# Kernel optimization log

Measured on AMD Instinct MI355X. Metric: run time of the kernel, lower is better.

Reference implementation:

```python
import jax, jax.numpy as jnp
import numpy as np
from functools import partial

# ---- constants from params ----
NODES = 64          # cfg_s[0]: nodes per graph
HEADS, BASES = 8, 4 # EGConv num_heads / num_bases (aggregators = ['symnorm'], A=1)
THRESH, LENS = 0.5, 0.5
ENC_THRESH, ENC_LENS = 0.5, 0.5
DECAY = 0.2
LSTM_ALPHA = 2.0

# ---- surrogate spike functions ----
@partial(jax.custom_vjp, nondiff_argnums=(1, 2))
def atan_spike(x, thresh, alpha):
    return (x > thresh).astype(x.dtype)

def _atan_fwd(x, thresh, alpha):
    return atan_spike(x, thresh, alpha), x

def _atan_bwd(thresh, alpha, x, g):
    grad = (alpha / 2.0) / (1.0 + (jnp.pi / 2.0 * alpha * (x - thresh)) ** 2)
    return (g * grad,)

atan_spike.defvjp(_atan_fwd, _atan_bwd)

@partial(jax.custom_vjp, nondiff_argnums=(1,))
def erf_spike(x, alpha):
    return (x > 0).astype(x.dtype)

def _erf_fwd(x, alpha):
    return erf_spike(x, alpha), x

def _erf_bwd(alpha, x, g):
    grad = alpha / (2.0 * jnp.sqrt(jnp.pi)) * jnp.exp(-(alpha * x / 2.0) ** 2)
    return (g * grad,)

erf_spike.defvjp(_erf_fwd, _erf_bwd)


def setup_inputs() -> dict:
    key = jax.random.key(0)
    N, Cin, T = 16384, 8, 32
    Cenc, Cgnn = 128, 128
    Fh = Cgnn // HEADS
    HID, FC1, NC = 512, 256, 4
    E = 262144
    ks = jax.random.split(key, 12)

    def w(k, shape, fan_in):
        return jax.random.normal(k, shape, jnp.float32) / np.float32(np.sqrt(fan_in))

    return {
        "x": jax.random.normal(ks[0], (N, Cin, T), jnp.float32),
        "edge_index": jax.random.randint(ks[1], (2, E), 0, N, dtype=jnp.int32),
        "enc_W": w(ks[2], (Cin, Cenc), Cin),
        "enc_b": jnp.zeros((Cenc,), jnp.float32),
        "bases_W": w(ks[3], (Cenc, BASES * Fh), Cenc),
        "bases_b": jnp.zeros((BASES * Fh,), jnp.float32),
        "comb_W": w(ks[4], (Cenc, HEADS * BASES), Cenc),
        "comb_b": jnp.zeros((HEADS * BASES,), jnp.float32),
        "conv_bias": jnp.zeros((Cgnn,), jnp.float32),
        "W_ih": w(ks[5], (NODES * Cgnn, 4 * HID), NODES * Cgnn),
        "W_hh": w(ks[6], (HID, 4 * HID), HID),
        "b_ih": jnp.zeros((4 * HID,), jnp.float32),
        "b_hh": jnp.zeros((4 * HID,), jnp.float32),
        "fc1_W": w(ks[7], (HID, FC1), HID),
        "fc1_b": jnp.zeros((FC1,), jnp.float32),
        "fc2_W": w(ks[8], (FC1, NC), FC1),
        "fc2_b": jnp.zeros((NC,), jnp.float32),
    }


def reference(x, edge_index, enc_W, enc_b, bases_W, bases_b, comb_W, comb_b,
              conv_bias, W_ih, W_hh, b_ih, b_hh, fc1_W, fc1_b, fc2_W, fc2_b):
    N, Cin, T = x.shape
    S = N // NODES
    Cgnn = conv_bias.shape[0]
    Fh = Cgnn // HEADS
    HID = W_hh.shape[0]
    FC1 = fc1_b.shape[0]
    NC = fc2_b.shape[0]

    # EGConv symnorm graph structure with self-loops (fixed across time)
    loop = jnp.arange(N, dtype=edge_index.dtype)
    s_all = jnp.concatenate([edge_index[0], loop])
    d_all = jnp.concatenate([edge_index[1], loop])
    deg = jax.ops.segment_sum(jnp.ones(s_all.shape[0], x.dtype), d_all, num_segments=N)
    dinv = jnp.where(deg > 0, jax.lax.rsqrt(jnp.maximum(deg, 1e-12)), 0.0)
    ew = dinv[s_all] * dinv[d_all]  # [E+N]

    xs = jnp.moveaxis(x, -1, 0)  # [T, N, Cin]

    def step(carry, xt):
        (enc_mem, enc_spike, c1_mem, c1_spike, lh, lc,
         h1_mem, h1_spike, h2_mem, h2_spike, h2_sum) = carry
        # encoding LIF
        enc_mem = enc_mem * DECAY * (1.0 - enc_spike) + xt @ enc_W + enc_b
        enc_spike = atan_spike(enc_mem, ENC_THRESH, ENC_LENS)
        # EGConv (symnorm aggregator, A=1)
        bases = enc_spike @ bases_W + bases_b                       # [N, B*Fh]
        agg = jax.ops.segment_sum(ew[:, None] * bases[s_all], d_all, num_segments=N)
        comb = (enc_spike @ comb_W + comb_b).reshape(N, HEADS, BASES)
        conv = jnp.einsum('nhb,nbf->nhf', comb, agg.reshape(N, BASES, Fh))
        conv = conv.reshape(S, NODES, Cgnn) + conv_bias
        # conv LIF
        c1_mem = c1_mem * DECAY * (1.0 - c1_spike) + conv
        c1_spike = atan_spike(c1_mem, THRESH, LENS)
        # spiking LSTM cell (erf surrogates on all gates)
        xl = c1_spike.reshape(S, NODES * Cgnn)
        gates = xl @ W_ih + b_ih + lh @ W_hh + b_hh
        i, f, g, o = jnp.split(gates, 4, axis=-1)
        i = erf_spike(i, LSTM_ALPHA)
        f = erf_spike(f, LSTM_ALPHA)
        g = erf_spike(g, LSTM_ALPHA)
        o = erf_spike(o, LSTM_ALPHA)
        lc = f * lc + i * g
        lh = lc * o
        # fc1 LIF
        h1_mem = h1_mem * DECAY * (1.0 - h1_spike) + lh @ fc1_W + fc1_b
        h1_spike = atan_spike(h1_mem, THRESH, LENS)
        # fc2 LIF
        h2_mem = h2_mem * DECAY * (1.0 - h2_spike) + h1_spike @ fc2_W + fc2_b
        h2_spike = atan_spike(h2_mem, THRESH, LENS)
        return (enc_mem, enc_spike, c1_mem, c1_spike, lh, lc,
                h1_mem, h1_spike, h2_mem, h2_spike, h2_sum + h2_spike), None

    Cenc = enc_b.shape[0]
    z = lambda shape: jnp.zeros(shape, x.dtype)
    carry0 = (z((N, Cenc)), z((N, Cenc)), z((S, NODES, Cgnn)), z((S, NODES, Cgnn)),
              z((S, HID)), z((S, HID)), z((S, FC1)), z((S, FC1)),
              z((S, NC)), z((S, NC)), z((S, NC)))
    carry, _ = jax.lax.scan(step, carry0, xs)
    h2_sum = carry[-1]
    return h2_sum / jnp.asarray(T, x.dtype)
```

## Files before the change

### kernel.cpp

```cpp
#include <hip/hip_runtime.h>

#define NN      16384
#define TSTEPS  32
#define SG      256
#define NE      262144
#define NPANEL  24
#define GSTRIDE 524288u

#define OFF_ENC_MEM   0u
#define OFF_ENC_SPK   2097152u
#define OFF_C1_MEM    4194304u
#define OFF_C1_SPK    6291456u
#define OFF_LH        8388608u
#define OFF_LC        8519680u
#define OFF_H1_MEM    8650752u
#define OFF_H1_SPK    8716288u
#define OFF_H2_MEM    8781824u
#define OFF_H2_SPK    8782848u
#define OFF_H2_SUM    8783872u
#define ZERO_FLOATS   8784896u
#define OFF_BASES     8784896u
#define OFF_COMB      9833472u
#define OFF_GATES     10357760u
#define OFF_PART      10882048u
#define OFF_DINV      23464960u
#define OFF_COLW      23481344u
#define FLOAT_END     23743488u
#define IOFF_DEG      0
#define IOFF_FILL     16384
#define IOFF_ROWPTR   32768
#define IOFF_EID      49153
#define IOFF_COL      311297
#define INT_COUNT     573441

__global__ void k_deg(const int* __restrict__ ei, int* __restrict__ deg) {
  int e = blockIdx.x * 256 + threadIdx.x;
  if (e < NE) atomicAdd(&deg[ei[NE + e]], 1);
}

__global__ void k_dinv(const int* __restrict__ deg, float* __restrict__ dinv) {
  int n = blockIdx.x * 256 + threadIdx.x;
  if (n < NN) dinv[n] = __fdiv_rn(1.0f, __fsqrt_rn((float)(deg[n] + 1)));
}

__global__ void k_scan(const int* __restrict__ deg, int* __restrict__ rowp) {
  __shared__ int sdata[1024];
  int tid = threadIdx.x;
  int base = tid * 16;
  int loc[16];
  int sum = 0;
  #pragma unroll
  for (int i = 0; i < 16; ++i) { loc[i] = sum; sum += deg[base + i]; }
  sdata[tid] = sum;
  __syncthreads();
  for (int off = 1; off < 1024; off <<= 1) {
    int v = 0;
    if (tid >= off) v = sdata[tid - off];
    __syncthreads();
    sdata[tid] += v;
    __syncthreads();
  }
  int excl = (tid == 0) ? 0 : sdata[tid - 1];
  #pragma unroll
  for (int i = 0; i < 16; ++i) rowp[base + i] = excl + loc[i];
  if (tid == 1023) rowp[NN] = sdata[1023];
}

__global__ void k_scatter(const int* __restrict__ ei, const int* __restrict__ rowp,
                          int* __restrict__ fill, int* __restrict__ eid) {
  int e = blockIdx.x * 256 + threadIdx.x;
  if (e >= NE) return;
  int d = ei[NE + e];
  int pos = rowp[d] + atomicAdd(&fill[d], 1);
  eid[pos] = e;
}

__global__ void k_sortadj(const int* __restrict__ rowp, int* __restrict__ eid,
                          const int* __restrict__ ei, const float* __restrict__ dinv,
                          int* __restrict__ col, float* __restrict__ colw) {
  int d = blockIdx.x * 256 + threadIdx.x;
  if (d >= NN) return;
  int r0 = rowp[d], r1 = rowp[d + 1];
  for (int i = r0 + 1; i < r1; ++i) {
    int key = eid[i];
    int j = i - 1;
    while (j >= r0 && eid[j] > key) { eid[j + 1] = eid[j]; --j; }
    eid[j + 1] = key;
  }
  for (int i = r0; i < r1; ++i) {
    int s = ei[eid[i]];
    col[i] = s;
    colw[i] = dinv[s];
  }
}

__global__ __launch_bounds__(256) void k_enc(
    const float* __restrict__ x, const float* __restrict__ encW, const float* __restrict__ encB,
    float* __restrict__ enc_mem, float* __restrict__ enc_spk, int t) {
  __shared__ float xs[2][8];
  int tid = threadIdx.x;
  int nb = blockIdx.x * 2;
  if (tid < 16)
    xs[tid >> 3][tid & 7] = x[(size_t)(nb + (tid >> 3)) * 256 + (size_t)(tid & 7) * 32 + t];
  __syncthreads();
  int nl = tid >> 7, j = tid & 127;
  int idx = (nb + nl) * 128 + j;
  float dot = 0.f;
  #pragma unroll
  for (int c = 0; c < 8; ++c) dot = __fmaf_rn(xs[nl][c], encW[c * 128 + j], dot);
  float m = enc_mem[idx], s = enc_spk[idx];
  float nm = __fadd_rn(__fadd_rn(__fmul_rn(__fmul_rn(m, 0.2f), __fsub_rn(1.f, s)), dot), encB[j]);
  enc_mem[idx] = nm;
  enc_spk[idx] = nm > 0.5f ? 1.f : 0.f;
}

__global__ __launch_bounds__(256) void k_bases_comb(
    const float* __restrict__ enc_spk,
    const float* __restrict__ basesW, const float* __restrict__ basesB,
    const float* __restrict__ combW, const float* __restrict__ combB,
    float* __restrict__ bases, float* __restrict__ comb) {
  __shared__ float sp[64 * 129];
  __shared__ float ob[64 * 65];
  __shared__ float oc[64 * 33];
  const int tid = threadIdx.x;
  const int nb = blockIdx.x * 64;
  #pragma unroll 4
  for (int k = 0; k < 32; ++k) {
    int idx = k * 256 + tid;
    int n = idx >> 7, j = idx & 127;
    sp[n * 129 + j] = enc_spk[(size_t)nb * 128 + idx];
  }
  __syncthreads();
  const int lane = tid & 63;
  const int w = tid >> 6;
  const float* spn = sp + lane * 129;
  if (w < 2) {
    const int ch0 = w * 32;
    const float* Wp = basesW + ch0;
    float acc[32];
    #pragma unroll
    for (int c = 0; c < 32; ++c) acc[c] = 0.f;
    for (int j = 0; j < 128; ++j) {
      const float s = spn[j];
      const float* wr = Wp + j * 64;
      #pragma unroll
      for (int c = 0; c < 32; ++c) acc[c] = __fmaf_rn(s, wr[c], acc[c]);
    }
    #pragma unroll
    for (int c = 0; c < 32; ++c) ob[lane * 65 + ch0 + c] = acc[c];
  } else {
    const int ch0 = (w - 2) * 16;
    const float* Wp = combW + ch0;
    float acc[16];
    #pragma unroll
    for (int c = 0; c < 16; ++c) acc[c] = 0.f;
    for (int j = 0; j < 128; ++j) {
      const float s = spn[j];
      const float* wr = Wp + j * 32;
      #pragma unroll
      for (int c = 0; c < 16; ++c) acc[c] = __fmaf_rn(s, wr[c], acc[c]);
    }
    #pragma unroll
    for (int c = 0; c < 16; ++c) oc[lane * 33 + ch0 + c] = acc[c];
  }
  __syncthreads();
  #pragma unroll
  for (int r = 0; r < 16; ++r) {
    int idx = r * 256 + tid;
    int n = idx >> 6, ch = idx & 63;
    bases[(size_t)(nb + n) * 64 + ch] = __fadd_rn(ob[n * 65 + ch], basesB[ch]);
  }
  #pragma unroll
  for (int r = 0; r < 8; ++r) {
    int idx = r * 256 + tid;
    int n = idx >> 5, ch = idx & 31;
    comb[(size_t)(nb + n) * 32 + ch] = __fadd_rn(oc[n * 33 + ch], combB[ch]);
  }
}

__global__ __launch_bounds__(256) void k_aggconv(
    const float* __restrict__ bases, const float* __restrict__ comb,
    const float* __restrict__ dinv, const int* __restrict__ rowp,
    const int* __restrict__ col, const float* __restrict__ colw,
    const float* __restrict__ convB,
    float* __restrict__ c1_mem, float* __restrict__ c1_spk) {
  __shared__ float aggl[4][64];
  __shared__ float combl[4][32];
  int w = threadIdx.x >> 6;
  int m = threadIdx.x & 63;
  int d = blockIdx.x * 4 + w;
  float dd = dinv[d];
  int r0 = rowp[d], r1 = rowp[d + 1];
  float acc = 0.f;
  for (int r = r0; r < r1; ++r) {
    int s = col[r];
    float ew  = __fmul_rn(colw[r], dd);
    float upd = __fmul_rn(ew, bases[(size_t)s * 64 + m]);
    acc = __fadd_rn(acc, upd);
  }
  {
    float ew  = __fmul_rn(dd, dd);
    float upd = __fmul_rn(ew, bases[(size_t)d * 64 + m]);
    acc = __fadd_rn(acc, upd);
  }
  aggl[w][m] = acc;
  if (m < 32) combl[w][m] = comb[(size_t)d * 32 + m];
  __syncthreads();
  #pragma unroll
  for (int half = 0; half < 2; ++half) {
    int j = m + half * 64;
    int h = j >> 4, f = j & 15;
    float cv = 0.f;
    #pragma unroll
    for (int b = 0; b < 4; ++b)
      cv = __fadd_rn(cv, __fmul_rn(combl[w][h * 4 + b], aggl[w][b * 16 + f]));
    cv = __fadd_rn(cv, convB[j]);
    int idx = d * 128 + j;
    float cm = c1_mem[idx], cs = c1_spk[idx];
    float nm = __fadd_rn(__fmul_rn(__fmul_rn(cm, 0.2f), __fsub_rn(1.f, cs)), cv);
    c1_mem[idx] = nm;
    c1_spk[idx] = nm > 0.5f ? 1.f : 0.f;
  }
}

__global__ __launch_bounds__(256) void k_gpanel(
    const float* __restrict__ xl, const float* __restrict__ lh,
    const float* __restrict__ Wih, const float* __restrict__ Whh,
    float* __restrict__ part) {
  __shared__ __align__(16) float Ast[16][132];
  __shared__ __align__(16) float Bs[16][132];
  const int tid = threadIdx.x;
  const int tx = tid & 15, ty = tid >> 4;
  const int n0 = blockIdx.x * 128;
  const int m0 = blockIdx.y * 128;
  const int z  = blockIdx.z;

  const float* Asrc; const float* Bsrc; int lda, k0, klen;
  if (z < 22) { Asrc = xl; Bsrc = Wih; lda = 8192; k0 = z * 384; klen = (z == 21) ? 128 : 384; }
  else        { Asrc = lh; Bsrc = Whh; lda = 512;  k0 = (z == 22) ? 0 : 384; klen = (z == 22) ? 384 : 128; }

  float acc[8][8];
  #pragma unroll
  for (int i = 0; i < 8; ++i)
    #pragma unroll
    for (int j = 0; j < 8; ++j) acc[i][j] = 0.f;

  const int arow = tid >> 1;
  const int acol = (tid & 1) * 8;
  const int brow = tid >> 5;
  const int bcol = (tid & 31) * 4;

  const int nkt = klen >> 4;
  for (int kt = 0; kt < nkt; ++kt) {
    const int kb = k0 + (kt << 4);
    __syncthreads();
    {
      const float* src = Asrc + (size_t)(m0 + arow) * lda + kb + acol;
      const float4 v0 = ((const float4*)src)[0];
      const float4 v1 = ((const float4*)src)[1];
      Ast[acol + 0][arow] = v0.x; Ast[acol + 1][arow] = v0.y;
      Ast[acol + 2][arow] = v0.z; Ast[acol + 3][arow] = v0.w;
      Ast[acol + 4][arow] = v1.x; Ast[acol + 5][arow] = v1.y;
      Ast[acol + 6][arow] = v1.z; Ast[acol + 7][arow] = v1.w;
    }
    {
      *(float4*)&Bs[brow][bcol] =
          *(const float4*)(Bsrc + (size_t)(kb + brow) * 2048 + n0 + bcol);
      *(float4*)&Bs[brow + 8][bcol] =
          *(const float4*)(Bsrc + (size_t)(kb + brow + 8) * 2048 + n0 + bcol);
    }
    __syncthreads();
    #pragma unroll
    for (int kk = 0; kk < 16; ++kk) {
      const float4 a0 = *(const float4*)&Ast[kk][ty * 4];
      const float4 a1 = *(const float4*)&Ast[kk][64 + ty * 4];
      const float4 b0 = *(const float4*)&Bs[kk][tx * 4];
      const float4 b1 = *(const float4*)&Bs[kk][64 + tx * 4];
      const float av[8] = {a0.x, a0.y, a0.z, a0.w, a1.x, a1.y, a1.z, a1.w};
      const float bv[8] = {b0.x, b0.y, b0.z, b0.w, b1.x, b1.y, b1.z, b1.w};
      #pragma unroll
      for (int i = 0; i < 8; ++i)
        #pragma unroll
        for (int j = 0; j < 8; ++j)
          acc[i][j] = __fmaf_rn(av[i], bv[j], acc[i][j]);
    }
  }
  float* dstz = part + (size_t)z * GSTRIDE + (size_t)m0 * 2048 + n0;
  #pragma unroll
  for (int i = 0; i < 8; ++i) {
    const int mr = ((i >> 2) << 6) + ty * 4 + (i & 3);
    float* row = dstz + (size_t)mr * 2048;
    *(float4*)(row + tx * 4)      = make_float4(acc[i][0], acc[i][1], acc[i][2], acc[i][3]);
    *(float4*)(row + 64 + tx * 4) = make_float4(acc[i][4], acc[i][5], acc[i][6], acc[i][7]);
  }
}

__global__ __launch_bounds__(256) void k_combine(
    const float* __restrict__ part, const float* __restrict__ bih,
    const float* __restrict__ bhh, float* __restrict__ gates) {
  const int idx = blockIdx.x * 256 + threadIdx.x;
  const float* p = part + idx;
  float tih = p[0];
  #pragma unroll
  for (int zz = 1; zz < 22; ++zz) tih = __fadd_rn(tih, p[(size_t)zz * GSTRIDE]);
  const float thh = __fadd_rn(p[22u * GSTRIDE], p[23u * GSTRIDE]);
  const int u = idx & 2047;
  gates[idx] = __fadd_rn(__fadd_rn(__fadd_rn(tih, bih[u]), thh), bhh[u]);
}

__global__ __launch_bounds__(256) void k_cell(
    const float* __restrict__ gates,
    float* __restrict__ lc, float* __restrict__ lh,
    const float* __restrict__ fc1W, const float* __restrict__ fc1b,
    const float* __restrict__ fc2W, const float* __restrict__ fc2b,
    float* __restrict__ h1_mem, float* __restrict__ h1_spk,
    float* __restrict__ h2_mem, float* __restrict__ h2_spk, float* __restrict__ h2_sum) {
  __shared__ float lhl[512];
  __shared__ float sp1l[256];
  const int s = blockIdx.x;
  const int p = threadIdx.x;
  #pragma unroll
  for (int half = 0; half < 2; ++half) {
    const int h = p + half * 256;
    const float giv = gates[(size_t)s * 2048 + h];
    const float gfv = gates[(size_t)s * 2048 + 512 + h];
    const float ggv = gates[(size_t)s * 2048 + 1024 + h];
    const float gov = gates[(size_t)s * 2048 + 1536 + h];
    const float iv = giv > 0.f ? 1.f : 0.f;
    const float fv = gfv > 0.f ? 1.f : 0.f;
    const float gv = ggv > 0.f ? 1.f : 0.f;
    const float ov = gov > 0.f ? 1.f : 0.f;
    const int li = s * 512 + h;
    const float lcv = __fadd_rn(__fmul_rn(fv, lc[li]), __fmul_rn(iv, gv));
    lc[li] = lcv;
    const float lhv = __fmul_rn(lcv, ov);
    lh[li] = lhv;
    lhl[h] = lhv;
  }
  __syncthreads();
  float a0 = 0.f, a1 = 0.f;
  #pragma unroll 8
  for (int q = 0; q < 384; ++q) a0 = __fmaf_rn(lhl[q], fc1W[q * 256 + p], a0);
  #pragma unroll 8
  for (int q = 384; q < 512; ++q) a1 = __fmaf_rn(lhl[q], fc1W[q * 256 + p], a1);
  const float dot1 = __fadd_rn(a0, a1);
  const int i1 = s * 256 + p;
  const float m1 = h1_mem[i1], s1o = h1_spk[i1];
  const float nm1 = __fadd_rn(__fadd_rn(__fmul_rn(__fmul_rn(m1, 0.2f), __fsub_rn(1.f, s1o)), dot1), fc1b[p]);
  h1_mem[i1] = nm1;
  const float sp1 = nm1 > 0.5f ? 1.f : 0.f;
  h1_spk[i1] = sp1;
  sp1l[p] = sp1;
  __syncthreads();
  if (p < 4) {
    float acc = 0.f;
    for (int q = 0; q < 256; ++q) acc = __fmaf_rn(sp1l[q], fc2W[q * 4 + p], acc);
    const int i2 = s * 4 + p;
    const float m2 = h2_mem[i2], s2o = h2_spk[i2];
    const float nm2 = __fadd_rn(__fadd_rn(__fmul_rn(__fmul_rn(m2, 0.2f), __fsub_rn(1.f, s2o)), acc), fc2b[p]);
    h2_mem[i2] = nm2;
    const float sp2 = nm2 > 0.5f ? 1.f : 0.f;
    h2_spk[i2] = sp2;
    h2_sum[i2] = __fadd_rn(h2_sum[i2], sp2);
  }
}

__global__ void k_out(const float* __restrict__ h2_sum, float* __restrict__ out) {
  int i = blockIdx.x * 256 + threadIdx.x;
  if (i < SG * 4) out[i] = __fmul_rn(h2_sum[i], 0.03125f);
}

extern "C" void kernel_launch(void* const* d_in, const int* in_sizes, int n_in,
                              void* d_out, int out_size, void* d_ws, size_t ws_size,
                              hipStream_t stream) {
  const float* x      = (const float*)d_in[0];
  const int*   ei     = (const int*)  d_in[1];
  const float* encW   = (const float*)d_in[2];
  const float* encB   = (const float*)d_in[3];
  const float* basesW = (const float*)d_in[4];
  const float* basesB = (const float*)d_in[5];
  const float* combW  = (const float*)d_in[6];
  const float* combB  = (const float*)d_in[7];
  const float* convB  = (const float*)d_in[8];
  const float* Wih    = (const float*)d_in[9];
  const float* Whh    = (const float*)d_in[10];
  const float* bih    = (const float*)d_in[11];
  const float* bhh    = (const float*)d_in[12];
  const float* fc1W   = (const float*)d_in[13];
  const float* fc1b   = (const float*)d_in[14];
  const float* fc2W   = (const float*)d_in[15];
  const float* fc2b   = (const float*)d_in[16];

  float* ws = (float*)d_ws;
  float* enc_mem = ws + OFF_ENC_MEM;
  float* enc_spk = ws + OFF_ENC_SPK;
  float* c1_mem  = ws + OFF_C1_MEM;
  float* c1_spk  = ws + OFF_C1_SPK;
  float* lhp     = ws + OFF_LH;
  float* lcp     = ws + OFF_LC;
  float* h1_mem  = ws + OFF_H1_MEM;
  float* h1_spk  = ws + OFF_H1_SPK;
  float* h2_mem  = ws + OFF_H2_MEM;
  float* h2_spk  = ws + OFF_H2_SPK;
  float* h2_sum  = ws + OFF_H2_SUM;
  float* bases   = ws + OFF_BASES;
  float* comb    = ws + OFF_COMB;
  float* gates   = ws + OFF_GATES;
  float* partp   = ws + OFF_PART;
  float* dinv    = ws + OFF_DINV;
  float* colw    = ws + OFF_COLW;
  int* ibase = (int*)((char*)d_ws + (size_t)FLOAT_END * 4);
  int* deg  = ibase + IOFF_DEG;
  int* fill = ibase + IOFF_FILL;
  int* rowp = ibase + IOFF_ROWPTR;
  int* eid  = ibase + IOFF_EID;
  int* col  = ibase + IOFF_COL;

  hipMemsetAsync(ws, 0, (size_t)ZERO_FLOATS * 4, stream);
  hipMemsetAsync(ibase, 0, 32768 * 4, stream);

  k_deg    <<<NE / 256, 256, 0, stream>>>(ei, deg);
  k_dinv   <<<NN / 256, 256, 0, stream>>>(deg, dinv);
  k_scan   <<<1, 1024, 0, stream>>>(deg, rowp);
  k_scatter<<<NE / 256, 256, 0, stream>>>(ei, rowp, fill, eid);
  k_sortadj<<<NN / 256, 256, 0, stream>>>(rowp, eid, ei, dinv, col, colw);

  for (int t = 0; t < TSTEPS; ++t) {
    k_enc       <<<NN / 2, 256, 0, stream>>>(x, encW, encB, enc_mem, enc_spk, t);
    k_bases_comb<<<NN / 64, 256, 0, stream>>>(enc_spk, basesW, basesB, combW, combB, bases, comb);
    k_aggconv   <<<NN / 4, 256, 0, stream>>>(bases, comb, dinv, rowp, col, colw, convB, c1_mem, c1_spk);
    k_gpanel    <<<dim3(16, 2, NPANEL), 256, 0, stream>>>(c1_spk, lhp, Wih, Whh, partp);
    k_combine   <<<2048, 256, 0, stream>>>(partp, bih, bhh, gates);
    k_cell      <<<SG, 256, 0, stream>>>(gates, lcp, lhp, fc1W, fc1b, fc2W, fc2b,
                                         h1_mem, h1_spk, h2_mem, h2_spk, h2_sum);
  }
  k_out<<<4, 256, 0, stream>>>(h2_sum, (float*)d_out);
}
```

Measured before the change: 7.218 ms.

## Fuse encoder LIF into bases kernel and stream GEMM B tiles through registers

The encoder LIF update now runs inside the bases/comb kernel. The spikes are written straight into shared memory, which removes one launch per timestep and a global re-read of enc_spk. The gate GEMM panel kernel now loads the W tiles directly from global memory into registers per thread instead of staging them in shared memory. It also halves the K tile to 8 and adds an occupancy hint of 3 blocks. This cuts LDS use and traffic, but each thread issues more uncoalesced-pattern global loads, the loop has more barrier iterations, and register pressure may rise.

```diff
diff --git a/kernel.cpp b/kernel.cpp
--- a/kernel.cpp
+++ b/kernel.cpp
@@ -94,41 +94,39 @@
   }
 }
 
-__global__ __launch_bounds__(256) void k_enc(
+__global__ __launch_bounds__(256) void k_encbases(
     const float* __restrict__ x, const float* __restrict__ encW, const float* __restrict__ encB,
-    float* __restrict__ enc_mem, float* __restrict__ enc_spk, int t) {
-  __shared__ float xs[2][8];
-  int tid = threadIdx.x;
-  int nb = blockIdx.x * 2;
-  if (tid < 16)
-    xs[tid >> 3][tid & 7] = x[(size_t)(nb + (tid >> 3)) * 256 + (size_t)(tid & 7) * 32 + t];
-  __syncthreads();
-  int nl = tid >> 7, j = tid & 127;
-  int idx = (nb + nl) * 128 + j;
-  float dot = 0.f;
-  #pragma unroll
-  for (int c = 0; c < 8; ++c) dot = __fmaf_rn(xs[nl][c], encW[c * 128 + j], dot);
-  float m = enc_mem[idx], s = enc_spk[idx];
-  float nm = __fadd_rn(__fadd_rn(__fmul_rn(__fmul_rn(m, 0.2f), __fsub_rn(1.f, s)), dot), encB[j]);
-  enc_mem[idx] = nm;
-  enc_spk[idx] = nm > 0.5f ? 1.f : 0.f;
-}
-
-__global__ __launch_bounds__(256) void k_bases_comb(
-    const float* __restrict__ enc_spk,
+    float* __restrict__ enc_mem, float* __restrict__ enc_spk,
     const float* __restrict__ basesW, const float* __restrict__ basesB,
     const float* __restrict__ combW, const float* __restrict__ combB,
-    float* __restrict__ bases, float* __restrict__ comb) {
+    float* __restrict__ bases, float* __restrict__ comb, int t) {
+  __shared__ float xs[64][8];
   __shared__ float sp[64 * 129];
   __shared__ float ob[64 * 65];
   __shared__ float oc[64 * 33];
   const int tid = threadIdx.x;
   const int nb = blockIdx.x * 64;
+  #pragma unroll
+  for (int r = 0; r < 2; ++r) {
+    int idx = r * 256 + tid;
+    int n = idx >> 3, c = idx & 7;
+    xs[n][c] = x[(size_t)(nb + n) * 256 + (size_t)c * 32 + t];
+  }
+  __syncthreads();
   #pragma unroll 4
   for (int k = 0; k < 32; ++k) {
     int idx = k * 256 + tid;
     int n = idx >> 7, j = idx & 127;
-    sp[n * 129 + j] = enc_spk[(size_t)nb * 128 + idx];
+    float dot = 0.f;
+    #pragma unroll
+    for (int c = 0; c < 8; ++c) dot = __fmaf_rn(xs[n][c], encW[c * 128 + j], dot);
+    size_t gi = (size_t)nb * 128 + idx;
+    float m = enc_mem[gi], s = enc_spk[gi];
+    float nm = __fadd_rn(__fadd_rn(__fmul_rn(__fmul_rn(m, 0.2f), __fsub_rn(1.f, s)), dot), encB[j]);
+    enc_mem[gi] = nm;
+    float spike = nm > 0.5f ? 1.f : 0.f;
+    enc_spk[gi] = spike;
+    sp[n * 129 + j] = spike;
   }
   __syncthreads();
   const int lane = tid & 63;
@@ -223,12 +221,11 @@
   }
 }
 
-__global__ __launch_bounds__(256) void k_gpanel(
+__global__ __launch_bounds__(256, 3) void k_gpanel(
     const float* __restrict__ xl, const float* __restrict__ lh,
     const float* __restrict__ Wih, const float* __restrict__ Whh,
     float* __restrict__ part) {
-  __shared__ __align__(16) float Ast[16][132];
-  __shared__ __align__(16) float Bs[16][132];
+  __shared__ __align__(16) float Ast[8][132];
   const int tid = threadIdx.x;
   const int tx = tid & 15, ty = tid >> 4;
   const int n0 = blockIdx.x * 128;
@@ -246,38 +243,32 @@
     for (int j = 0; j < 8; ++j) acc[i][j] = 0.f;
 
   const int arow = tid >> 1;
-  const int acol = (tid & 1) * 8;
-  const int brow = tid >> 5;
-  const int bcol = (tid & 31) * 4;
-
-  const int nkt = klen >> 4;
+  const int acol = (tid & 1) * 4;
+
+  const int nkt = klen >> 3;
   for (int kt = 0; kt < nkt; ++kt) {
-    const int kb = k0 + (kt << 4);
+    const int kb = k0 + (kt << 3);
+    float4 b0r[8], b1r[8];
+    const float* bp = Bsrc + (size_t)kb * 2048 + n0 + tx * 4;
+    #pragma unroll
+    for (int kk = 0; kk < 8; ++kk) {
+      b0r[kk] = *(const float4*)(bp + kk * 2048);
+      b1r[kk] = *(const float4*)(bp + kk * 2048 + 64);
+    }
     __syncthreads();
     {
-      const float* src = Asrc + (size_t)(m0 + arow) * lda + kb + acol;
-      const float4 v0 = ((const float4*)src)[0];
-      const float4 v1 = ((const float4*)src)[1];
-      Ast[acol + 0][arow] = v0.x; Ast[acol + 1][arow] = v0.y;
-      Ast[acol + 2][arow] = v0.z; Ast[acol + 3][arow] = v0.w;
-      Ast[acol + 4][arow] = v1.x; Ast[acol + 5][arow] = v1.y;
-      Ast[acol + 6][arow] = v1.z; Ast[acol + 7][arow] = v1.w;
-    }
-    {
-      *(float4*)&Bs[brow][bcol] =
-          *(const float4*)(Bsrc + (size_t)(kb + brow) * 2048 + n0 + bcol);
-      *(float4*)&Bs[brow + 8][bcol] =
-          *(const float4*)(Bsrc + (size_t)(kb + brow + 8) * 2048 + n0 + bcol);
+      const float4 v = *(const float4*)(Asrc + (size_t)(m0 + arow) * lda + kb + acol);
+      Ast[acol + 0][arow] = v.x; Ast[acol + 1][arow] = v.y;
+      Ast[acol + 2][arow] = v.z; Ast[acol + 3][arow] = v.w;
     }
     __syncthreads();
     #pragma unroll
-    for (int kk = 0; kk < 16; ++kk) {
+    for (int kk = 0; kk < 8; ++kk) {
       const float4 a0 = *(const float4*)&Ast[kk][ty * 4];
       const float4 a1 = *(const float4*)&Ast[kk][64 + ty * 4];
-      const float4 b0 = *(const float4*)&Bs[kk][tx * 4];
-      const float4 b1 = *(const float4*)&Bs[kk][64 + tx * 4];
       const float av[8] = {a0.x, a0.y, a0.z, a0.w, a1.x, a1.y, a1.z, a1.w};
-      const float bv[8] = {b0.x, b0.y, b0.z, b0.w, b1.x, b1.y, b1.z, b1.w};
+      const float bv[8] = {b0r[kk].x, b0r[kk].y, b0r[kk].z, b0r[kk].w,
+                           b1r[kk].x, b1r[kk].y, b1r[kk].z, b1r[kk].w};
       #pragma unroll
       for (int i = 0; i < 8; ++i)
         #pragma unroll
@@ -426,13 +417,13 @@
   k_sortadj<<<NN / 256, 256, 0, stream>>>(rowp, eid, ei, dinv, col, colw);
 
   for (int t = 0; t < TSTEPS; ++t) {
-    k_enc       <<<NN / 2, 256, 0, stream>>>(x, encW, encB, enc_mem, enc_spk, t);
-    k_bases_comb<<<NN / 64, 256, 0, stream>>>(enc_spk, basesW, basesB, combW, combB, bases, comb);
-    k_aggconv   <<<NN / 4, 256, 0, stream>>>(bases, comb, dinv, rowp, col, colw, convB, c1_mem, c1_spk);
-    k_gpanel    <<<dim3(16, 2, NPANEL), 256, 0, stream>>>(c1_spk, lhp, Wih, Whh, partp);
-    k_combine   <<<2048, 256, 0, stream>>>(partp, bih, bhh, gates);
-    k_cell      <<<SG, 256, 0, stream>>>(gates, lcp, lhp, fc1W, fc1b, fc2W, fc2b,
-                                         h1_mem, h1_spk, h2_mem, h2_spk, h2_sum);
+    k_encbases<<<NN / 64, 256, 0, stream>>>(x, encW, encB, enc_mem, enc_spk,
+                                            basesW, basesB, combW, combB, bases, comb, t);
+    k_aggconv <<<NN / 4, 256, 0, stream>>>(bases, comb, dinv, rowp, col, colw, convB, c1_mem, c1_spk);
+    k_gpanel  <<<dim3(16, 2, NPANEL), 256, 0, stream>>>(c1_spk, lhp, Wih, Whh, partp);
+    k_combine <<<2048, 256, 0, stream>>>(partp, bih, bhh, gates);
+    k_cell    <<<SG, 256, 0, stream>>>(gates, lcp, lhp, fc1W, fc1b, fc2W, fc2b,
+                                       h1_mem, h1_spk, h2_mem, h2_spk, h2_sum);
   }
   k_out<<<4, 256, 0, stream>>>(h2_sum, (float*)d_out);
 }
```

Measured after the change: 7.959 ms. 10.3% more time.
